# Kernel tuning notes

Measured on AMD Instinct MI355X. Metric: run time of the kernel, lower is better.

## Reference

```python
import jax, jax.numpy as jnp
import numpy as np

DIM = 768
NUM_HEADS = 16
HEAD_DIM = DIM // NUM_HEADS
SCALE = HEAD_DIM ** -0.5


def setup_inputs() -> dict:
    key = jax.random.key(0)
    ks = jax.random.split(key, 5)
    B, S = 2, 2048
    x = jax.random.normal(ks[0], (B, S, DIM), dtype=jnp.float32)
    # nn.Linear(dim, dim, bias=False): weight shape [out, in]; y = x @ W.T
    init = 1.0 / np.sqrt(DIM)
    Wq = jax.random.uniform(ks[1], (DIM, DIM), jnp.float32, -init, init)
    Wk = jax.random.uniform(ks[2], (DIM, DIM), jnp.float32, -init, init)
    Wv = jax.random.uniform(ks[3], (DIM, DIM), jnp.float32, -init, init)
    Wo = jax.random.uniform(ks[4], (DIM, DIM), jnp.float32, -init, init)
    return {"x": x, "Wq": Wq, "Wk": Wk, "Wv": Wv, "Wo": Wo}


def reference(x, Wq, Wk, Wv, Wo):
    B, S, _ = x.shape
    # projections (torch Linear: x @ W.T)
    q = jnp.einsum('bsd,ed->bse', x, Wq).reshape(B, S, NUM_HEADS, HEAD_DIM)
    k = jnp.einsum('bsd,ed->bse', x, Wk).reshape(B, S, NUM_HEADS, HEAD_DIM)
    v = jnp.einsum('bsd,ed->bse', x, Wv).reshape(B, S, NUM_HEADS, HEAD_DIM)
    # [B, H, S, S] scores, stable softmax, then context
    scores = jnp.einsum('bqhd,bkhd->bhqk', q, k) * SCALE
    probs = jax.nn.softmax(scores, axis=-1)  # dropout is identity in eval
    ctx = jnp.einsum('bhqk,bkhd->bqhd', probs, v).reshape(B, S, DIM)
    return jnp.einsum('bsd,ed->bse', ctx, Wo)
```

## Files before the change

kernel.cpp:

```cpp
#include <hip/hip_runtime.h>
#include <cstdint>

#define DIM 768
#define SEQ 2048
#define NB 2
#define NH 16
#define HD 48
#define NROWS (NB*SEQ)

typedef __attribute__((ext_vector_type(8))) short bf16x8;
typedef __attribute__((ext_vector_type(4))) float f32x4;
typedef __attribute__((ext_vector_type(16))) float f32x16;
typedef unsigned int u32;

__device__ __forceinline__ short f2bf(float f) {
    union { float f; uint32_t u; } v; v.f = f;
    uint32_t u = v.u;
    uint32_t r = (u + 0x7FFFu + ((u >> 16) & 1u)) >> 16;
    return (short)r;
}
__device__ __forceinline__ u32 cvtpk(float lo, float hi) {
    u32 r;
    asm("v_cvt_pk_bf16_f32 %0, %1, %2" : "=v"(r) : "v"(lo), "v"(hi));
    return r;
}

__device__ __forceinline__ void gload16(const short* g, short* l) {
    __builtin_amdgcn_global_load_lds(
        (const __attribute__((address_space(1))) void*)g,
        (__attribute__((address_space(3))) void*)l, 16, 0, 0);
}

__global__ __launch_bounds__(256)
void cvt_bf16(const float* __restrict__ x,  const float* __restrict__ wq,
              const float* __restrict__ wk, const float* __restrict__ wv,
              const float* __restrict__ wo, short* __restrict__ dst)
{
    const int XN4 = (NROWS*DIM)/4;
    const int WN4 = (DIM*DIM)/4;
    const int T4  = XN4 + 4*WN4;
    for (int i = blockIdx.x*blockDim.x + threadIdx.x; i < T4; i += gridDim.x*blockDim.x) {
        const float* src; int off;
        if (i < XN4) { src = x; off = i; }
        else {
            int j = i - XN4;
            int w = j / WN4, r = j - w*WN4;
            src = (w==0) ? wq : (w==1) ? wk : (w==2) ? wv : wo;
            off = r;
        }
        float4 v = *(const float4*)(src + (size_t)off*4);
        short4 s; s.x=f2bf(v.x); s.y=f2bf(v.y); s.z=f2bf(v.z); s.w=f2bf(v.w);
        *(short4*)(dst + (size_t)i*4) = s;
    }
}

template<bool OUT_F32>
__global__ __launch_bounds__(256)
void gemm_gl(const short* __restrict__ A, const short* __restrict__ B,
             void* __restrict__ C0v, void* __restrict__ C1v, void* __restrict__ C2v)
{
    __shared__ short As[128*64];
    __shared__ short Bs[96*64];

    const int tid  = threadIdx.x;
    const int lane = tid & 63;
    const int wid  = tid >> 6;
    const int wr = wid >> 1, wc = wid & 1;
    const int m  = lane & 15, kb = lane >> 4;
    const int m0 = blockIdx.y * 128, n0 = blockIdx.x * 96;
    const int lr = lane >> 3, lsl = lane & 7;
    const int gsl = (lsl ^ lr) * 8;

    void* Cv = C0v;
    const int slice = n0 / DIM;
    if (slice == 1) Cv = C1v; else if (slice == 2) Cv = C2v;
    const int ncol0 = n0 - slice * DIM;

    f32x4 acc[4][3];
#pragma unroll
    for (int i = 0; i < 4; ++i)
#pragma unroll
        for (int j = 0; j < 3; ++j) acc[i][j] = (f32x4){0.f,0.f,0.f,0.f};

    for (int kt = 0; kt < DIM/64; ++kt) {
        const int k0 = kt * 64;
        __syncthreads();
#pragma unroll
        for (int i = 0; i < 4; ++i) {
            int r0 = wid*32 + i*8;
            gload16(&A[(size_t)(m0 + r0 + lr)*DIM + k0 + gsl], &As[r0*64]);
        }
#pragma unroll
        for (int i = 0; i < 3; ++i) {
            int r0 = wid*24 + i*8;
            gload16(&B[(size_t)(n0 + r0 + lr)*DIM + k0 + gsl], &Bs[r0*64]);
        }
        __syncthreads();

        bf16x8 af[2][4], bfr[2][3];
#pragma unroll
        for (int t = 0; t < 2; ++t) {
            int sl = ((t*4 + kb) ^ (m & 7)) * 8;
#pragma unroll
            for (int f = 0; f < 4; ++f)
                af[t][f]  = *(const bf16x8*)&As[(wr*64 + f*16 + m)*64 + sl];
#pragma unroll
            for (int f = 0; f < 3; ++f)
                bfr[t][f] = *(const bf16x8*)&Bs[(wc*48 + f*16 + m)*64 + sl];
        }
#pragma unroll
        for (int fm = 0; fm < 4; ++fm)
#pragma unroll
            for (int fn = 0; fn < 3; ++fn) {
                acc[fm][fn] = __builtin_amdgcn_mfma_f32_16x16x32_bf16(af[0][fm], bfr[0][fn], acc[fm][fn], 0, 0, 0);
                acc[fm][fn] = __builtin_amdgcn_mfma_f32_16x16x32_bf16(af[1][fm], bfr[1][fn], acc[fm][fn], 0, 0, 0);
            }
    }

#pragma unroll
    for (int fm = 0; fm < 4; ++fm)
#pragma unroll
        for (int fn = 0; fn < 3; ++fn) {
            int col = ncol0 + wc*48 + fn*16 + m;
#pragma unroll
            for (int r = 0; r < 4; ++r) {
                int row = m0 + wr*64 + fm*16 + kb*4 + r;
                if (OUT_F32)
                    ((float*)Cv)[(size_t)row*DIM + col] = acc[fm][fn][r];
                else
                    ((short*)Cv)[(size_t)row*DIM + col] = f2bf(acc[fm][fn][r]);
            }
        }
}

__global__ __launch_bounds__(256)
void flash2(const short* __restrict__ Qb, const short* __restrict__ Kb,
            const short* __restrict__ Vb, short* __restrict__ Ctx)
{
    __shared__ short K_lds[64*64];
    __shared__ short Vt_lds[64*68];

    const int tid  = threadIdx.x;
    const int wid  = tid >> 6, lane = tid & 63;
    const int r    = lane & 31, hi = lane >> 5;
    const size_t base = (size_t)blockIdx.z*SEQ*DIM + (size_t)blockIdx.y*HD;
    const int q0 = blockIdx.x*128 + wid*32;
    const float C2  = 0.20823688f;
    const float THR = 11.5f;

    for (int i = tid; i < 16*68; i += 256) Vt_lds[48*68 + i] = 0;

    bf16x8 qf[3];
#pragma unroll
    for (int s = 0; s < 3; ++s)
        qf[s] = *(const bf16x8*)&Qb[base + (size_t)(q0 + r)*DIM + s*16 + hi*8];

    f32x16 z16;
#pragma unroll
    for (int i = 0; i < 16; ++i) z16[i] = 0.f;

    f32x16 acc0 = z16, acc1 = z16;
    float m_i = -1e30f, l_i = 0.f;

    const int row0 = tid >> 3,       ps0 = tid & 7;
    const int row1 = (tid+256) >> 3, ps1 = tid & 7;
    const int ls0 = ps0 ^ (row0 & 7), ls1 = ps1 ^ (row1 & 7);

    bf16x8 k0r, k1r; short vreg[12];
    k0r = *(const bf16x8*)&Kb[base + (size_t)row0*DIM + ls0*8];
    k1r = *(const bf16x8*)&Kb[base + (size_t)row1*DIM + ls1*8];
#pragma unroll
    for (int j = 0; j < 12; ++j)
        vreg[j] = Vb[base + (size_t)lane*DIM + wid*12 + j];

    for (int t = 0; t < SEQ/64; ++t) {
        __syncthreads();
        *(bf16x8*)&K_lds[row0*64 + ps0*8] = k0r;
        *(bf16x8*)&K_lds[row1*64 + ps1*8] = k1r;
#pragma unroll
        for (int j = 0; j < 12; ++j)
            Vt_lds[(wid*12 + j)*68 + lane] = vreg[j];
        __syncthreads();

        if (t + 1 < SEQ/64) {
            int c0 = (t+1)*64;
            k0r = *(const bf16x8*)&Kb[base + (size_t)(c0 + row0)*DIM + ls0*8];
            k1r = *(const bf16x8*)&Kb[base + (size_t)(c0 + row1)*DIM + ls1*8];
#pragma unroll
            for (int j = 0; j < 12; ++j)
                vreg[j] = Vb[base + (size_t)(c0 + lane)*DIM + wid*12 + j];
        }

        f32x16 sa[2];
#pragma unroll
        for (int ct = 0; ct < 2; ++ct) {
            f32x16 a = z16;
#pragma unroll
            for (int s = 0; s < 3; ++s) {
                int row = ct*32 + r;
                bf16x8 kf = *(const bf16x8*)&K_lds[row*64 + ((s*2+hi) ^ (row&7))*8];
                a = __builtin_amdgcn_mfma_f32_32x32x16_bf16(kf, qf[s], a, 0, 0, 0);
            }
            sa[ct] = a;
        }

        float mx = -1e30f;
#pragma unroll
        for (int ct = 0; ct < 2; ++ct)
#pragma unroll
            for (int i = 0; i < 16; ++i) mx = fmaxf(mx, sa[ct][i]);
        mx = fmaxf(mx, __shfl_xor(mx, 32));
        mx *= C2;

        float mn = m_i;
        if (!__all(mx - m_i <= THR)) {
            mn = fmaxf(m_i, mx);
            float al = exp2f(m_i - mn);
            l_i *= al;
#pragma unroll
            for (int i = 0; i < 16; ++i) { acc0[i] *= al; acc1[i] *= al; }
            m_i = mn;
        }

        float rs = 0.f;
        u32 w[2][8], sw[2][8];
#pragma unroll
        for (int ct = 0; ct < 2; ++ct)
#pragma unroll
            for (int k = 0; k < 8; ++k) {
                float p0 = exp2f(fmaf(sa[ct][2*k],   C2, -mn));
                float p1 = exp2f(fmaf(sa[ct][2*k+1], C2, -mn));
                w[ct][k] = cvtpk(p0, p1);
                rs += p0 + p1;
            }
        rs += __shfl_xor(rs, 32);
        l_i += rs;
#pragma unroll
        for (int ct = 0; ct < 2; ++ct)
#pragma unroll
            for (int k = 0; k < 8; ++k) sw[ct][k] = (u32)__shfl_xor((int)w[ct][k], 32);

#pragma unroll
        for (int ct = 0; ct < 2; ++ct)
#pragma unroll
            for (int hf = 0; hf < 2; ++hf) {
                u32 f0 = hi ? sw[ct][4*hf+2] : w[ct][4*hf+0];
                u32 f1 = hi ? sw[ct][4*hf+3] : w[ct][4*hf+1];
                u32 f2 = hi ? w[ct][4*hf+2]  : sw[ct][4*hf+0];
                u32 f3 = hi ? w[ct][4*hf+3]  : sw[ct][4*hf+1];
                int4 pw = make_int4((int)f0, (int)f1, (int)f2, (int)f3);
                bf16x8 pb = __builtin_bit_cast(bf16x8, pw);
#pragma unroll
                for (int dt = 0; dt < 2; ++dt) {
                    int off = (dt*32 + r)*68 + ct*32 + hf*16 + hi*8;
                    short4 v0 = *(const short4*)&Vt_lds[off];
                    short4 v1 = *(const short4*)&Vt_lds[off + 4];
                    bf16x8 av = {v0.x, v0.y, v0.z, v0.w, v1.x, v1.y, v1.z, v1.w};
                    if (dt == 0) acc0 = __builtin_amdgcn_mfma_f32_32x32x16_bf16(av, pb, acc0, 0, 0, 0);
                    else         acc1 = __builtin_amdgcn_mfma_f32_32x32x16_bf16(av, pb, acc1, 0, 0, 0);
                }
            }
    }

    float inv = 1.0f / l_i;
#pragma unroll
    for (int g = 0; g < 16; ++g) {
        int d = (g&3) + 8*(g>>2) + 4*hi;
        Ctx[base + (size_t)(q0 + r)*DIM + d] = f2bf(acc0[g] * inv);
    }
#pragma unroll
    for (int g = 0; g < 8; ++g) {
        int d = 32 + (g&3) + 8*(g>>2) + 4*hi;
        Ctx[base + (size_t)(q0 + r)*DIM + d] = f2bf(acc1[g] * inv);
    }
}

extern "C" void kernel_launch(void* const* d_in, const int* in_sizes, int n_in,
                              void* d_out, int out_size, void* d_ws, size_t ws_size,
                              hipStream_t stream)
{
    const float* x  = (const float*)d_in[0];
    const float* Wq = (const float*)d_in[1];
    const float* Wk = (const float*)d_in[2];
    const float* Wv = (const float*)d_in[3];
    const float* Wo = (const float*)d_in[4];
    float* out = (float*)d_out;

    const size_t XN = (size_t)NROWS * DIM;
    const size_t WN = (size_t)DIM * DIM;

    short* xb   = (short*)d_ws;
    short* wcat = xb   + XN;
    short* wob  = wcat + 3*WN;
    short* qb   = wob  + WN;
    short* kbuf = qb   + XN;
    short* vbuf = kbuf + XN;
    short* ctxb = vbuf + XN;

    cvt_bf16<<<1024, 256, 0, stream>>>(x, Wq, Wk, Wv, Wo, xb);

    dim3 g1(3*DIM/96, NROWS/128, 1);
    gemm_gl<false><<<g1, 256, 0, stream>>>(xb, wcat, qb, kbuf, vbuf);

    dim3 g2(SEQ/128, NH, NB);
    flash2<<<g2, 256, 0, stream>>>(qb, kbuf, vbuf, ctxb);

    dim3 g3(DIM/96, NROWS/128, 1);
    gemm_gl<true><<<g3, 256, 0, stream>>>(ctxb, wob, out, out, out);
}
```

Baseline: 181.2 us.

## Double-buffer GEMM LDS tiles with async prefetch of the next K slice

Both projection GEMMs now keep two LDS buffers of K=32 slices and issue the global-to-LDS loads for the next slice before computing on the current one. Each iteration needs one barrier instead of two. The aim is to overlap global memory latency with MFMA work. In exchange the K step is halved, so there are twice as many iterations and barriers, and the LDS swizzle changes to a 4-slot XOR pattern.

```diff
diff --git a/kernel.cpp b/kernel.cpp
--- a/kernel.cpp
+++ b/kernel.cpp
@@ -56,11 +56,11 @@
 
 template<bool OUT_F32>
 __global__ __launch_bounds__(256)
-void gemm_gl(const short* __restrict__ A, const short* __restrict__ B,
-             void* __restrict__ C0v, void* __restrict__ C1v, void* __restrict__ C2v)
+void gemm_pipe(const short* __restrict__ A, const short* __restrict__ B,
+               void* __restrict__ C0v, void* __restrict__ C1v, void* __restrict__ C2v)
 {
-    __shared__ short As[128*64];
-    __shared__ short Bs[96*64];
+    __shared__ short As[2][128*32];
+    __shared__ short Bs[2][96*32];
 
     const int tid  = threadIdx.x;
     const int lane = tid & 63;
@@ -68,8 +68,8 @@
     const int wr = wid >> 1, wc = wid & 1;
     const int m  = lane & 15, kb = lane >> 4;
     const int m0 = blockIdx.y * 128, n0 = blockIdx.x * 96;
-    const int lr = lane >> 3, lsl = lane & 7;
-    const int gsl = (lsl ^ lr) * 8;
+    const int lr  = lane >> 2;
+    const int gsl = ((lane & 3) ^ (lr & 3)) * 8;
 
     void* Cv = C0v;
     const int slice = n0 / DIM;
@@ -82,40 +82,41 @@
 #pragma unroll
         for (int j = 0; j < 3; ++j) acc[i][j] = (f32x4){0.f,0.f,0.f,0.f};
 
-    for (int kt = 0; kt < DIM/64; ++kt) {
-        const int k0 = kt * 64;
+#define STAGE(buf, k0)                                                        \
+    for (int c = wid; c < 14; c += 4) {                                       \
+        if (c < 8)                                                            \
+            gload16(&A[(size_t)(m0 + c*16 + lr)*DIM + (k0) + gsl],            \
+                    &As[buf][c*512]);                                         \
+        else                                                                  \
+            gload16(&B[(size_t)(n0 + (c-8)*16 + lr)*DIM + (k0) + gsl],        \
+                    &Bs[buf][(c-8)*512]);                                     \
+    }
+
+    STAGE(0, 0);
+
+    for (int kt = 0; kt < DIM/32; ++kt) {
+        const int cur = kt & 1;
         __syncthreads();
-#pragma unroll
-        for (int i = 0; i < 4; ++i) {
-            int r0 = wid*32 + i*8;
-            gload16(&A[(size_t)(m0 + r0 + lr)*DIM + k0 + gsl], &As[r0*64]);
-        }
-#pragma unroll
-        for (int i = 0; i < 3; ++i) {
-            int r0 = wid*24 + i*8;
-            gload16(&B[(size_t)(n0 + r0 + lr)*DIM + k0 + gsl], &Bs[r0*64]);
-        }
-        __syncthreads();
-
-        bf16x8 af[2][4], bfr[2][3];
-#pragma unroll
-        for (int t = 0; t < 2; ++t) {
-            int sl = ((t*4 + kb) ^ (m & 7)) * 8;
-#pragma unroll
-            for (int f = 0; f < 4; ++f)
-                af[t][f]  = *(const bf16x8*)&As[(wr*64 + f*16 + m)*64 + sl];
-#pragma unroll
-            for (int f = 0; f < 3; ++f)
-                bfr[t][f] = *(const bf16x8*)&Bs[(wc*48 + f*16 + m)*64 + sl];
+        if (kt + 1 < DIM/32) STAGE(cur ^ 1, (kt+1)*32);
+
+        bf16x8 af[4], bfr[3];
+#pragma unroll
+        for (int f = 0; f < 4; ++f) {
+            int row = wr*64 + f*16 + m;
+            af[f] = *(const bf16x8*)&As[cur][row*32 + ((kb ^ (m & 3)) << 3)];
+        }
+#pragma unroll
+        for (int f = 0; f < 3; ++f) {
+            int row = wc*48 + f*16 + m;
+            bfr[f] = *(const bf16x8*)&Bs[cur][row*32 + ((kb ^ (m & 3)) << 3)];
         }
 #pragma unroll
         for (int fm = 0; fm < 4; ++fm)
 #pragma unroll
-            for (int fn = 0; fn < 3; ++fn) {
-                acc[fm][fn] = __builtin_amdgcn_mfma_f32_16x16x32_bf16(af[0][fm], bfr[0][fn], acc[fm][fn], 0, 0, 0);
-                acc[fm][fn] = __builtin_amdgcn_mfma_f32_16x16x32_bf16(af[1][fm], bfr[1][fn], acc[fm][fn], 0, 0, 0);
-            }
-    }
+            for (int fn = 0; fn < 3; ++fn)
+                acc[fm][fn] = __builtin_amdgcn_mfma_f32_16x16x32_bf16(af[fm], bfr[fn], acc[fm][fn], 0, 0, 0);
+    }
+#undef STAGE
 
 #pragma unroll
     for (int fm = 0; fm < 4; ++fm)
@@ -300,11 +301,11 @@
     cvt_bf16<<<1024, 256, 0, stream>>>(x, Wq, Wk, Wv, Wo, xb);
 
     dim3 g1(3*DIM/96, NROWS/128, 1);
-    gemm_gl<false><<<g1, 256, 0, stream>>>(xb, wcat, qb, kbuf, vbuf);
+    gemm_pipe<false><<<g1, 256, 0, stream>>>(xb, wcat, qb, kbuf, vbuf);
 
     dim3 g2(SEQ/128, NH, NB);
     flash2<<<g2, 256, 0, stream>>>(qb, kbuf, vbuf, ctxb);
 
     dim3 g3(DIM/96, NROWS/128, 1);
-    gemm_gl<true><<<g3, 256, 0, stream>>>(ctxb, wob, out, out, out);
-}
+    gemm_pipe<true><<<g3, 256, 0, stream>>>(ctxb, wob, out, out, out);
+}
```

After: 190.3 us. +5.0%, slower.

## Split attention KV range in two with combine kernel; shrink output GEMM tile

Applied to the files above, without the earlier changes.

The attention kernel now splits the key/value sequence into two halves across blockIdx.z. Each half writes unnormalized partial outputs along with its running max and sum, and a new combine kernel merges them with log-sum-exp weights. This doubles the attention grid from 512 to 1024 blocks to fill the GPU's CUs better. The output-projection GEMM uses a 64-row tile to double its block count. The cost is an extra launch, extra partial-output traffic, and a bf16 rounding of the unnormalized partials.

```diff
diff --git a/kernel.cpp b/kernel.cpp
--- a/kernel.cpp
+++ b/kernel.cpp
@@ -18,6 +18,9 @@
     uint32_t u = v.u;
     uint32_t r = (u + 0x7FFFu + ((u >> 16) & 1u)) >> 16;
     return (short)r;
+}
+__device__ __forceinline__ float bf2f(short s) {
+    return __uint_as_float(((u32)(unsigned short)s) << 16);
 }
 __device__ __forceinline__ u32 cvtpk(float lo, float hi) {
     u32 r;
@@ -54,20 +57,21 @@
     }
 }
 
-template<bool OUT_F32>
+template<int MT, bool OUT_F32>
 __global__ __launch_bounds__(256)
 void gemm_gl(const short* __restrict__ A, const short* __restrict__ B,
              void* __restrict__ C0v, void* __restrict__ C1v, void* __restrict__ C2v)
 {
-    __shared__ short As[128*64];
+    __shared__ short As[MT*64];
     __shared__ short Bs[96*64];
+    const int FM = MT/32;
 
     const int tid  = threadIdx.x;
     const int lane = tid & 63;
     const int wid  = tid >> 6;
     const int wr = wid >> 1, wc = wid & 1;
     const int m  = lane & 15, kb = lane >> 4;
-    const int m0 = blockIdx.y * 128, n0 = blockIdx.x * 96;
+    const int m0 = blockIdx.y * MT, n0 = blockIdx.x * 96;
     const int lr = lane >> 3, lsl = lane & 7;
     const int gsl = (lsl ^ lr) * 8;
 
@@ -76,9 +80,9 @@
     if (slice == 1) Cv = C1v; else if (slice == 2) Cv = C2v;
     const int ncol0 = n0 - slice * DIM;
 
-    f32x4 acc[4][3];
-#pragma unroll
-    for (int i = 0; i < 4; ++i)
+    f32x4 acc[FM][3];
+#pragma unroll
+    for (int i = 0; i < FM; ++i)
 #pragma unroll
         for (int j = 0; j < 3; ++j) acc[i][j] = (f32x4){0.f,0.f,0.f,0.f};
 
@@ -86,8 +90,8 @@
         const int k0 = kt * 64;
         __syncthreads();
 #pragma unroll
-        for (int i = 0; i < 4; ++i) {
-            int r0 = wid*32 + i*8;
+        for (int i = 0; i < FM; ++i) {
+            int r0 = wid*(MT/4) + i*8;
             gload16(&A[(size_t)(m0 + r0 + lr)*DIM + k0 + gsl], &As[r0*64]);
         }
 #pragma unroll
@@ -97,19 +101,19 @@
         }
         __syncthreads();
 
-        bf16x8 af[2][4], bfr[2][3];
+        bf16x8 af[2][FM], bfr[2][3];
 #pragma unroll
         for (int t = 0; t < 2; ++t) {
             int sl = ((t*4 + kb) ^ (m & 7)) * 8;
 #pragma unroll
-            for (int f = 0; f < 4; ++f)
-                af[t][f]  = *(const bf16x8*)&As[(wr*64 + f*16 + m)*64 + sl];
+            for (int f = 0; f < FM; ++f)
+                af[t][f]  = *(const bf16x8*)&As[(wr*(MT/2) + f*16 + m)*64 + sl];
 #pragma unroll
             for (int f = 0; f < 3; ++f)
                 bfr[t][f] = *(const bf16x8*)&Bs[(wc*48 + f*16 + m)*64 + sl];
         }
 #pragma unroll
-        for (int fm = 0; fm < 4; ++fm)
+        for (int fm = 0; fm < FM; ++fm)
 #pragma unroll
             for (int fn = 0; fn < 3; ++fn) {
                 acc[fm][fn] = __builtin_amdgcn_mfma_f32_16x16x32_bf16(af[0][fm], bfr[0][fn], acc[fm][fn], 0, 0, 0);
@@ -118,13 +122,13 @@
     }
 
 #pragma unroll
-    for (int fm = 0; fm < 4; ++fm)
+    for (int fm = 0; fm < FM; ++fm)
 #pragma unroll
         for (int fn = 0; fn < 3; ++fn) {
             int col = ncol0 + wc*48 + fn*16 + m;
 #pragma unroll
             for (int r = 0; r < 4; ++r) {
-                int row = m0 + wr*64 + fm*16 + kb*4 + r;
+                int row = m0 + wr*(MT/2) + fm*16 + kb*4 + r;
                 if (OUT_F32)
                     ((float*)Cv)[(size_t)row*DIM + col] = acc[fm][fn][r];
                 else
@@ -134,8 +138,9 @@
 }
 
 __global__ __launch_bounds__(256)
-void flash2(const short* __restrict__ Qb, const short* __restrict__ Kb,
-            const short* __restrict__ Vb, short* __restrict__ Ctx)
+void flash2s(const short* __restrict__ Qb, const short* __restrict__ Kb,
+             const short* __restrict__ Vb, short* __restrict__ Op,
+             float* __restrict__ Mp, float* __restrict__ Lp)
 {
     __shared__ short K_lds[64*64];
     __shared__ short Vt_lds[64*68];
@@ -143,8 +148,12 @@
     const int tid  = threadIdx.x;
     const int wid  = tid >> 6, lane = tid & 63;
     const int r    = lane & 31, hi = lane >> 5;
-    const size_t base = (size_t)blockIdx.z*SEQ*DIM + (size_t)blockIdx.y*HD;
+    const int b  = blockIdx.z >> 1, sp = blockIdx.z & 1;
+    const int h  = blockIdx.y;
+    const size_t base = (size_t)b*SEQ*DIM + (size_t)h*HD;
     const int q0 = blockIdx.x*128 + wid*32;
+    const int NT = SEQ/128;
+    const int T0 = sp * NT;
     const float C2  = 0.20823688f;
     const float THR = 11.5f;
 
@@ -167,13 +176,16 @@
     const int ls0 = ps0 ^ (row0 & 7), ls1 = ps1 ^ (row1 & 7);
 
     bf16x8 k0r, k1r; short vreg[12];
-    k0r = *(const bf16x8*)&Kb[base + (size_t)row0*DIM + ls0*8];
-    k1r = *(const bf16x8*)&Kb[base + (size_t)row1*DIM + ls1*8];
-#pragma unroll
-    for (int j = 0; j < 12; ++j)
-        vreg[j] = Vb[base + (size_t)lane*DIM + wid*12 + j];
-
-    for (int t = 0; t < SEQ/64; ++t) {
+    {
+        const int c0 = T0*64;
+        k0r = *(const bf16x8*)&Kb[base + (size_t)(c0 + row0)*DIM + ls0*8];
+        k1r = *(const bf16x8*)&Kb[base + (size_t)(c0 + row1)*DIM + ls1*8];
+#pragma unroll
+        for (int j = 0; j < 12; ++j)
+            vreg[j] = Vb[base + (size_t)(c0 + lane)*DIM + wid*12 + j];
+    }
+
+    for (int t = 0; t < NT; ++t) {
         __syncthreads();
         *(bf16x8*)&K_lds[row0*64 + ps0*8] = k0r;
         *(bf16x8*)&K_lds[row1*64 + ps1*8] = k1r;
@@ -182,8 +194,8 @@
             Vt_lds[(wid*12 + j)*68 + lane] = vreg[j];
         __syncthreads();
 
-        if (t + 1 < SEQ/64) {
-            int c0 = (t+1)*64;
+        if (t + 1 < NT) {
+            int c0 = (T0 + t + 1)*64;
             k0r = *(const bf16x8*)&Kb[base + (size_t)(c0 + row0)*DIM + ls0*8];
             k1r = *(const bf16x8*)&Kb[base + (size_t)(c0 + row1)*DIM + ls1*8];
 #pragma unroll
@@ -262,17 +274,47 @@
             }
     }
 
-    float inv = 1.0f / l_i;
+    const size_t prow = (size_t)(sp*NB + b)*SEQ + q0 + r;
+    const size_t pbase = prow*DIM + (size_t)h*HD;
 #pragma unroll
     for (int g = 0; g < 16; ++g) {
         int d = (g&3) + 8*(g>>2) + 4*hi;
-        Ctx[base + (size_t)(q0 + r)*DIM + d] = f2bf(acc0[g] * inv);
+        Op[pbase + d] = f2bf(acc0[g]);
     }
 #pragma unroll
     for (int g = 0; g < 8; ++g) {
         int d = 32 + (g&3) + 8*(g>>2) + 4*hi;
-        Ctx[base + (size_t)(q0 + r)*DIM + d] = f2bf(acc1[g] * inv);
-    }
+        Op[pbase + d] = f2bf(acc1[g]);
+    }
+    Mp[prow*NH + h] = m_i;
+    Lp[prow*NH + h] = l_i;
+}
+
+__global__ __launch_bounds__(256)
+void combine(const short* __restrict__ Op, const float* __restrict__ Mp,
+             const float* __restrict__ Lp, short* __restrict__ Ctx)
+{
+    int idx = blockIdx.x*256 + threadIdx.x;
+    int dc = idx % 6;
+    int h  = (idx / 6) & 15;
+    int bq = idx / 96;
+    size_t r0 = (size_t)bq, r1 = (size_t)NROWS + bq;
+    float m1 = Mp[r0*NH + h], m2 = Mp[r1*NH + h];
+    float l1 = Lp[r0*NH + h], l2 = Lp[r1*NH + h];
+    float m  = fmaxf(m1, m2);
+    float w1 = exp2f(m1 - m), w2 = exp2f(m2 - m);
+    float inv = 1.0f / (w1*l1 + w2*l2);
+    w1 *= inv; w2 *= inv;
+    size_t off = (size_t)h*HD + dc*8;
+    bf16x8 a = *(const bf16x8*)&Op[r0*DIM + off];
+    bf16x8 b = *(const bf16x8*)&Op[r1*DIM + off];
+    float o[8];
+#pragma unroll
+    for (int e = 0; e < 8; ++e)
+        o[e] = w1*bf2f(a[e]) + w2*bf2f(b[e]);
+    int4 pw = make_int4((int)cvtpk(o[0],o[1]), (int)cvtpk(o[2],o[3]),
+                        (int)cvtpk(o[4],o[5]), (int)cvtpk(o[6],o[7]));
+    *(bf16x8*)&Ctx[(size_t)bq*DIM + off] = __builtin_bit_cast(bf16x8, pw);
 }
 
 extern "C" void kernel_launch(void* const* d_in, const int* in_sizes, int n_in,
@@ -296,15 +338,20 @@
     short* kbuf = qb   + XN;
     short* vbuf = kbuf + XN;
     short* ctxb = vbuf + XN;
+    short* opart= ctxb + XN;
+    float* mpart= (float*)(opart + 2*XN);
+    float* lpart= mpart + (size_t)2*NROWS*NH;
 
     cvt_bf16<<<1024, 256, 0, stream>>>(x, Wq, Wk, Wv, Wo, xb);
 
     dim3 g1(3*DIM/96, NROWS/128, 1);
-    gemm_gl<false><<<g1, 256, 0, stream>>>(xb, wcat, qb, kbuf, vbuf);
-
-    dim3 g2(SEQ/128, NH, NB);
-    flash2<<<g2, 256, 0, stream>>>(qb, kbuf, vbuf, ctxb);
-
-    dim3 g3(DIM/96, NROWS/128, 1);
-    gemm_gl<true><<<g3, 256, 0, stream>>>(ctxb, wob, out, out, out);
-}
+    gemm_gl<128, false><<<g1, 256, 0, stream>>>(xb, wcat, qb, kbuf, vbuf);
+
+    dim3 g2(SEQ/128, NH, NB*2);
+    flash2s<<<g2, 256, 0, stream>>>(qb, kbuf, vbuf, opart, mpart, lpart);
+
+    combine<<<(NROWS*NH*6)/256, 256, 0, stream>>>(opart, mpart, lpart, ctxb);
+
+    dim3 g3(DIM/96, NROWS/64, 1);
+    gemm_gl<64, true><<<g3, 256, 0, stream>>>(ctxb, wob, out, out, out);
+}
```

Result: faster. 176.6 us (-2.6%).
